# Kernel tuning notes

Hardware: AMD Instinct MI355X
Metric: run time of the kernel (lower is better)

The kernel has to match this reference:

```python
import jax, jax.numpy as jnp
import numpy as np

N = 4_194_304          # number of samples
NUM_TIMES = 2048       # number of distinct (integer) event times


def setup_inputs() -> dict:
    key = jax.random.key(0)
    k1, k2, k3 = jax.random.split(key, 3)
    hazard_ratio = jax.random.normal(k1, (N, 1), dtype=jnp.float32)
    durations = jax.random.randint(k2, (N,), 0, NUM_TIMES, dtype=jnp.int32)
    events = jax.random.randint(k3, (N,), 0, 2, dtype=jnp.int32)
    return {"hazard_ratio": hazard_ratio, "durations": durations, "events": events}


def _cox_efron_loss(hazard_ratio, durations, events):
    """Vectorized Efron-tie Cox PH loss; same math as the nested-loop torch code.

    Original per unique event time t with n tied events:
        loss += sum_k hr_k  -  sum_{k=0}^{n-1} log( sum_{d_i>=t} e^{hr_i} - (k/n) * sum_{tied} e^{hr} )
    which we evaluate per-event-sample using its rank k among ties at its time.
    """
    hr = hazard_ratio.reshape(-1)                       # [N]  (squeeze(-1))
    e = events.astype(hr.dtype)                         # [N] 0/1 floats
    exp_hr = jnp.exp(hr)

    # Per-time aggregates (time ids are 0..NUM_TIMES-1)
    s = jax.ops.segment_sum(exp_hr, durations, num_segments=NUM_TIMES)        # sum e^hr at time d
    R = jnp.cumsum(s[::-1])[::-1]                                             # R[t] = sum_{d>=t} e^hr  (at-risk)
    T = jax.ops.segment_sum(exp_hr * e, durations, num_segments=NUM_TIMES)    # tied-event sum at time t
    n = jax.ops.segment_sum(e, durations, num_segments=NUM_TIMES)             # # tied events at time t

    # Rank of each event sample among the tied events at its time (0-indexed).
    order = jnp.argsort(durations)
    d_s = durations[order]
    e_s = e[order]
    cs = jnp.cumsum(e_s)                                # running event count
    is_start = jnp.concatenate([jnp.array([True]), d_s[1:] != d_s[:-1]])
    # cs - e_s at a segment start equals the event count before the segment;
    # carry it forward with a running max (offsets are nondecreasing, fillers are -1).
    start_val = jnp.where(is_start, cs - e_s, -1.0)
    offset = jax.lax.cummax(start_val)
    rank = cs - offset - 1.0                            # in {0..n-1} for event samples

    n_i = jnp.maximum(n[d_s], 1.0)                      # safe for non-event rows (masked below)
    corr = jnp.log(R[d_s] - (rank / n_i) * T[d_s])      # Efron correction term per event
    corr_sum = jnp.sum(jnp.where(e_s > 0, corr, 0.0))

    loss = jnp.sum(hr * e) - corr_sum
    return -loss / (jnp.sum(e) + 1e-7)


def reference(hazard_ratio, durations, events):
    return _cox_efron_loss(hazard_ratio, durations, events)
```

## Files before the change

kernel.cpp:

```cpp
#include <hip/hip_runtime.h>

#define NT 2048
#define HB 256
#define HT 1024
#define RB 256
#define RT 1024
#define EB 128
#define ET 1024

#define SC      4096.0f
#define INV_SC  (1.0 / 4096.0)
#define TM26    ((1u << 26) - 1)

typedef unsigned long long u64;
typedef unsigned u32;

__device__ __forceinline__ double wave_reduce(double v) {
#pragma unroll
    for (int o = 32; o > 0; o >>= 1) v += __shfl_down(v, o, 64);
    return v;
}

__global__ __launch_bounds__(HT) void k_hist(
    const float* __restrict__ hr, const int* __restrict__ dur,
    const int* __restrict__ ev, int n,
    u32* __restrict__ s0_part, u32* __restrict__ tn_part,
    double* __restrict__ hrE_part, double* __restrict__ eCnt_part,
    unsigned* __restrict__ counter)
{
    __shared__ u32    loc[2][2 * NT];
    __shared__ double redH[HT / 64], redC[HT / 64];

    const int tid = threadIdx.x, bid = blockIdx.x;
    if (bid == 0 && tid == 0) *counter = 0u;

    for (int i = tid; i < 2 * NT; i += HT) { loc[0][i] = 0u; loc[1][i] = 0u; }
    __syncthreads();

    u32* img = loc[(tid >> 6) & 1];

    float hrE = 0.f;
    int   ec  = 0;
    const int stride = HB * HT;
    const int nv = n >> 2;
    const float4* hr4 = (const float4*)hr;
    const int4*   d4p = (const int4*)dur;
    const int4*   e4p = (const int4*)ev;

    auto process = [&](const float4& h, const int4& d, const int4& e) {
        float hh[4] = { h.x, h.y, h.z, h.w };
        int   dd[4] = { d.x, d.y, d.z, d.w };
        int   ee[4] = { e.x, e.y, e.z, e.w };
        u32 val[4]; int idx[4];
#pragma unroll
        for (int u = 0; u < 4; ++u) {
            float eh = __expf(hh[u]);
            val[u] = (u32)(eh * SC + 0.5f) + ((u32)ee[u] << 26);
            idx[u] = dd[u] + (ee[u] << 11);
        }
#pragma unroll
        for (int u = 0; u < 4; ++u)
            atomicAdd(&img[idx[u]], val[u]);
#pragma unroll
        for (int u = 0; u < 4; ++u) {
            hrE += hh[u] * (float)ee[u];
            ec  += ee[u];
        }
    };

    int i = bid * HT + tid;
    if (i < nv) {
        float4 h_c = hr4[i];
        int4   d_c = d4p[i];
        int4   e_c = e4p[i];
        for (i += stride; i < nv; i += stride) {
            float4 h_n = hr4[i];
            int4   d_n = d4p[i];
            int4   e_n = e4p[i];
            process(h_c, d_c, e_c);
            h_c = h_n; d_c = d_n; e_c = e_n;
        }
        process(h_c, d_c, e_c);
    }
    for (int j = (nv << 2) + bid * HT + tid; j < n; j += stride) {
        float h = hr[j]; int d = dur[j]; int e = ev[j];
        float eh = __expf(h);
        atomicAdd(&loc[(tid >> 6) & 1][d + (e << 11)],
                  (u32)(eh * SC + 0.5f) + ((u32)e << 26));
        hrE += h * (float)e;
        ec  += e;
    }
    __syncthreads();

    const size_t base = (size_t)bid * NT;
    for (int k = tid; k < NT; k += HT) {
        s0_part[base + k] = loc[0][k] + loc[1][k];
        u32 a = loc[0][NT + k], b = loc[1][NT + k];
        tn_part[base + k] = (((a >> 26) + (b >> 26)) << 26)
                          + ((a & TM26) + (b & TM26));
    }

    double hrEd = wave_reduce((double)hrE);
    double ecd  = wave_reduce((double)ec);
    if ((tid & 63) == 0) { redH[tid >> 6] = hrEd; redC[tid >> 6] = ecd; }
    __syncthreads();
    if (tid == 0) {
        double hh = 0.0, cc = 0.0;
#pragma unroll
        for (int w = 0; w < HT / 64; ++w) { hh += redH[w]; cc += redC[w]; }
        hrE_part[bid]  = hh;
        eCnt_part[bid] = cc;
    }
}

__global__ __launch_bounds__(RT) void k_reduce(
    const u32* __restrict__ s0_part, const u32* __restrict__ tn_part,
    double* __restrict__ s_fin, double* __restrict__ T_fin,
    unsigned* __restrict__ n_fin)
{
    __shared__ u64      rs[128][8];
    __shared__ u64      rt[128][8];
    __shared__ unsigned rn[128][8];
    __shared__ u64      ps[8][2], pt[8][2];
    __shared__ unsigned pn[8][2];

    const int bi = threadIdx.x & 7;
    const int jg = threadIdx.x >> 3;
    const int t  = blockIdx.x * 8 + bi;

    u64 s = 0ull, T = 0ull;
    unsigned c = 0u;
#pragma unroll
    for (int m = 0; m < HB / 128; ++m) {
        int j = jg + (m << 7);
        size_t idx = (size_t)j * NT + t;
        s += s0_part[idx];
        u32 v = tn_part[idx];
        T += v & TM26;
        c += v >> 26;
    }
    rs[jg][bi] = s; rt[jg][bi] = T; rn[jg][bi] = c;
    __syncthreads();

    const int wv  = threadIdx.x >> 6;
    const int l   = threadIdx.x & 63;
    const int bin = wv >> 1;
    const int hf  = wv & 1;
    u64 S  = rs[hf * 64 + l][bin];
    u64 TT = rt[hf * 64 + l][bin];
    u64 C  = rn[hf * 64 + l][bin];
#pragma unroll
    for (int o = 32; o > 0; o >>= 1) {
        S  += __shfl_down(S,  o, 64);
        TT += __shfl_down(TT, o, 64);
        C  += __shfl_down(C,  o, 64);
    }
    if (l == 0) { ps[bin][hf] = S; pt[bin][hf] = TT; pn[bin][hf] = (unsigned)C; }
    __syncthreads();
    if (threadIdx.x < 8) {
        int b = threadIdx.x;
        u64 S2  = ps[b][0] + ps[b][1];
        u64 TT2 = pt[b][0] + pt[b][1];
        unsigned C2 = pn[b][0] + pn[b][1];
        int tt = blockIdx.x * 8 + b;
        s_fin[tt] = (double)(S2 + TT2) * INV_SC;
        T_fin[tt] = (double)TT2 * INV_SC;
        n_fin[tt] = C2;
    }
}

__global__ __launch_bounds__(ET) void k_scan_efron_final(
    const double* __restrict__ s_fin, const double* __restrict__ T_fin,
    const unsigned* __restrict__ n_fin,
    double* __restrict__ corr_part, const double* __restrict__ hrE_part,
    const double* __restrict__ eCnt_part,
    unsigned* __restrict__ counter, float* __restrict__ out)
{
    __shared__ double sa[NT];
    __shared__ double sb[NT];
    __shared__ double red[16];
    __shared__ unsigned is_last;

    const int tid = threadIdx.x, bid = blockIdx.x;

    for (int i = tid; i < NT; i += ET) sa[i] = s_fin[i];
    __syncthreads();
    double* cur = sa;
    double* nxt = sb;
    for (int off = 1; off < NT; off <<= 1) {
        for (int i = tid; i < NT; i += ET) {
            double v = cur[i];
            if (i + off < NT) v += cur[i + off];
            nxt[i] = v;
        }
        __syncthreads();
        double* tmp = cur; cur = nxt; nxt = tmp;
    }

    const int wv = tid >> 6;
    const int l  = tid & 63;
    const int t  = bid * 16 + wv;
    unsigned nt = n_fin[t];
    double acc = 0.0;
    if (nt > 0) {
        double Rt = cur[t];
        double Tt = T_fin[t];
        double inv = 1.0 / (double)nt;
        for (unsigned k = l; k < nt; k += 64)
            acc += (double)logf((float)(Rt - (double)k * inv * Tt));
    }
    acc = wave_reduce(acc);
    if (l == 0) red[wv] = acc;
    __syncthreads();
    if (tid == 0) {
        double c = 0.0;
#pragma unroll
        for (int m = 0; m < 16; ++m) c += red[m];
        corr_part[bid] = c;
    }
    __syncthreads();

    if (tid == 0) {
        __threadfence();
        unsigned ticket = atomicAdd(counter, 1u);
        is_last = (ticket == EB - 1) ? 1u : 0u;
    }
    __syncthreads();
    if (is_last) {
        __threadfence();
        __shared__ double redA[16], redB[16], redC[16];
        double a = (tid < EB) ? corr_part[tid] : 0.0;
        double h = 0.0, c = 0.0;
        if (tid < HB) { h = hrE_part[tid]; c = eCnt_part[tid]; }
        a = wave_reduce(a); h = wave_reduce(h); c = wave_reduce(c);
        if ((tid & 63) == 0) { redA[tid >> 6] = a; redB[tid >> 6] = h; redC[tid >> 6] = c; }
        __syncthreads();
        if (tid == 0) {
            double A = 0.0, H = 0.0, C = 0.0;
#pragma unroll
            for (int w = 0; w < 16; ++w) { A += redA[w]; H += redB[w]; C += redC[w]; }
            out[0] = (float)(-(H - A) / (C + 1e-7));
        }
    }
}

extern "C" void kernel_launch(void* const* d_in, const int* in_sizes, int n_in,
                              void* d_out, int out_size, void* d_ws, size_t ws_size,
                              hipStream_t stream)
{
    const float* hr  = (const float*)d_in[0];
    const int*   dur = (const int*)d_in[1];
    const int*   ev  = (const int*)d_in[2];
    int n = in_sizes[1];

    char* ws = (char*)d_ws;
    u32*      s0_part   = (u32*)ws;
    u32*      tn_part   = (u32*)(ws + (size_t)2 * 1024 * 1024);
    char*     p         = ws + (size_t)4 * 1024 * 1024;
    double*   s_fin     = (double*)p;          p += NT * 8;
    double*   T_fin     = (double*)p;          p += NT * 8;
    unsigned* n_fin     = (unsigned*)p;        p += NT * 4;
    double*   corr_part = (double*)p;          p += EB * 8;
    double*   hrE_part  = (double*)p;          p += HB * 8;
    double*   eCnt_part = (double*)p;          p += HB * 8;
    unsigned* counter   = (unsigned*)p;

    hipLaunchKernelGGL(k_hist, dim3(HB), dim3(HT), 0, stream,
                       hr, dur, ev, n, s0_part, tn_part, hrE_part, eCnt_part, counter);
    hipLaunchKernelGGL(k_reduce, dim3(RB), dim3(RT), 0, stream,
                       s0_part, tn_part, s_fin, T_fin, n_fin);
    hipLaunchKernelGGL(k_scan_efron_final, dim3(EB), dim3(ET), 0, stream,
                       s_fin, T_fin, n_fin, corr_part, hrE_part, eCnt_part,
                       counter, (float*)d_out);
}
```

Before: 35.71 us.

## Fuse reduce and scan kernels using per-block chunk sums for suffix offsets

The histogram kernel now also writes per-block sums over 128 chunks of 16 time bins. The separate reduce and scan+Efron kernels are merged into one finish kernel. Each of its 128 blocks reduces its own 16 bins across all partial histograms, builds a 128-entry suffix scan of chunk totals, and adds a local suffix within its chunk to get the at-risk sums. This removes one kernel launch, the intermediate global arrays, and the 2048-wide scan repeated in every block. The cost is an extra chunk reduction in the histogram kernel and a reduction over all chunk partials in every finish block.

After: 39.60 us. 1.11x slower.

```diff
diff --git a/kernel.cpp b/kernel.cpp
--- a/kernel.cpp
+++ b/kernel.cpp
@@ -3,10 +3,9 @@
 #define NT 2048
 #define HB 256
 #define HT 1024
-#define RB 256
-#define RT 1024
-#define EB 128
-#define ET 1024
+#define NC 128
+#define FB 128
+#define FT 1024
 
 #define SC      4096.0f
 #define INV_SC  (1.0 / 4096.0)
@@ -25,6 +24,7 @@
     const float* __restrict__ hr, const int* __restrict__ dur,
     const int* __restrict__ ev, int n,
     u32* __restrict__ s0_part, u32* __restrict__ tn_part,
+    u64* __restrict__ chunk_part,
     double* __restrict__ hrE_part, double* __restrict__ eCnt_part,
     unsigned* __restrict__ counter)
 {
@@ -100,6 +100,18 @@
                           + ((a & TM26) + (b & TM26));
     }
 
+    if (tid < NC) {
+        const int t0 = tid * (NT / NC);
+        u64 s = 0ull;
+#pragma unroll
+        for (int j = 0; j < NT / NC; ++j) {
+            int t = t0 + j;
+            s += (u64)loc[0][t] + (u64)loc[1][t]
+               + (u64)(loc[0][NT + t] & TM26) + (u64)(loc[1][NT + t] & TM26);
+        }
+        chunk_part[(size_t)bid * NC + tid] = s;
+    }
+
     double hrEd = wave_reduce((double)hrE);
     double ecd  = wave_reduce((double)ec);
     if ((tid & 63) == 0) { redH[tid >> 6] = hrEd; redC[tid >> 6] = ecd; }
@@ -113,104 +125,109 @@
     }
 }
 
-__global__ __launch_bounds__(RT) void k_reduce(
+__global__ __launch_bounds__(FT) void k_finish(
     const u32* __restrict__ s0_part, const u32* __restrict__ tn_part,
-    double* __restrict__ s_fin, double* __restrict__ T_fin,
-    unsigned* __restrict__ n_fin)
-{
-    __shared__ u64      rs[128][8];
-    __shared__ u64      rt[128][8];
-    __shared__ unsigned rn[128][8];
-    __shared__ u64      ps[8][2], pt[8][2];
-    __shared__ unsigned pn[8][2];
-
-    const int bi = threadIdx.x & 7;
-    const int jg = threadIdx.x >> 3;
-    const int t  = blockIdx.x * 8 + bi;
-
-    u64 s = 0ull, T = 0ull;
-    unsigned c = 0u;
-#pragma unroll
-    for (int m = 0; m < HB / 128; ++m) {
-        int j = jg + (m << 7);
-        size_t idx = (size_t)j * NT + t;
-        s += s0_part[idx];
-        u32 v = tn_part[idx];
-        T += v & TM26;
-        c += v >> 26;
-    }
-    rs[jg][bi] = s; rt[jg][bi] = T; rn[jg][bi] = c;
-    __syncthreads();
-
-    const int wv  = threadIdx.x >> 6;
-    const int l   = threadIdx.x & 63;
-    const int bin = wv >> 1;
-    const int hf  = wv & 1;
-    u64 S  = rs[hf * 64 + l][bin];
-    u64 TT = rt[hf * 64 + l][bin];
-    u64 C  = rn[hf * 64 + l][bin];
-#pragma unroll
-    for (int o = 32; o > 0; o >>= 1) {
-        S  += __shfl_down(S,  o, 64);
-        TT += __shfl_down(TT, o, 64);
-        C  += __shfl_down(C,  o, 64);
-    }
-    if (l == 0) { ps[bin][hf] = S; pt[bin][hf] = TT; pn[bin][hf] = (unsigned)C; }
-    __syncthreads();
-    if (threadIdx.x < 8) {
-        int b = threadIdx.x;
-        u64 S2  = ps[b][0] + ps[b][1];
-        u64 TT2 = pt[b][0] + pt[b][1];
-        unsigned C2 = pn[b][0] + pn[b][1];
-        int tt = blockIdx.x * 8 + b;
-        s_fin[tt] = (double)(S2 + TT2) * INV_SC;
-        T_fin[tt] = (double)TT2 * INV_SC;
-        n_fin[tt] = C2;
-    }
-}
-
-__global__ __launch_bounds__(ET) void k_scan_efron_final(
-    const double* __restrict__ s_fin, const double* __restrict__ T_fin,
-    const unsigned* __restrict__ n_fin,
-    double* __restrict__ corr_part, const double* __restrict__ hrE_part,
-    const double* __restrict__ eCnt_part,
+    const u64* __restrict__ chunk_part,
+    const double* __restrict__ hrE_part, const double* __restrict__ eCnt_part,
+    double* __restrict__ corr_part,
     unsigned* __restrict__ counter, float* __restrict__ out)
 {
-    __shared__ double sa[NT];
-    __shared__ double sb[NT];
+    __shared__ u64 rs[64][16];
+    __shared__ u64 rt[64][16];
+    __shared__ u32 rn[64][16];
+    __shared__ u64 sbin[16];
+    __shared__ u64 tbin[16];
+    __shared__ u32 nbin[16];
+    __shared__ u64 cstage[8][NC];
+    __shared__ u64 ctA[NC], ctB[NC];
+    __shared__ u64 Rfx[16];
     __shared__ double red[16];
     __shared__ unsigned is_last;
 
     const int tid = threadIdx.x, bid = blockIdx.x;
 
-    for (int i = tid; i < NT; i += ET) sa[i] = s_fin[i];
-    __syncthreads();
-    double* cur = sa;
-    double* nxt = sb;
-    for (int off = 1; off < NT; off <<= 1) {
-        for (int i = tid; i < NT; i += ET) {
-            double v = cur[i];
-            if (i + off < NT) v += cur[i + off];
-            nxt[i] = v;
-        }
-        __syncthreads();
-        double* tmp = cur; cur = nxt; nxt = tmp;
-    }
-
-    const int wv = tid >> 6;
-    const int l  = tid & 63;
-    const int t  = bid * 16 + wv;
-    unsigned nt = n_fin[t];
-    double acc = 0.0;
-    if (nt > 0) {
-        double Rt = cur[t];
-        double Tt = T_fin[t];
-        double inv = 1.0 / (double)nt;
-        for (unsigned k = l; k < nt; k += 64)
-            acc += (double)logf((float)(Rt - (double)k * inv * Tt));
-    }
-    acc = wave_reduce(acc);
-    if (l == 0) red[wv] = acc;
+    {
+        const int bi = tid & 15;
+        const int jg = tid >> 4;
+        const int t  = bid * 16 + bi;
+        u64 s = 0ull, T = 0ull; u32 c = 0u;
+#pragma unroll
+        for (int r = 0; r < 4; ++r) {
+            int row = jg * 4 + r;
+            size_t idx = (size_t)row * NT + t;
+            s += s0_part[idx];
+            u32 v = tn_part[idx];
+            T += v & TM26;
+            c += v >> 26;
+        }
+        rs[jg][bi] = s; rt[jg][bi] = T; rn[jg][bi] = c;
+    }
+    __syncthreads();
+    {
+        const int wv = tid >> 6;
+        const int l  = tid & 63;
+        u64 S = rs[l][wv], TT = rt[l][wv], C = rn[l][wv];
+#pragma unroll
+        for (int o = 32; o > 0; o >>= 1) {
+            S  += __shfl_down(S,  o, 64);
+            TT += __shfl_down(TT, o, 64);
+            C  += __shfl_down(C,  o, 64);
+        }
+        if (l == 0) { sbin[wv] = S + TT; tbin[wv] = TT; nbin[wv] = (u32)C; }
+    }
+
+    {
+        const int c = tid & (NC - 1);
+        const int g = tid >> 7;
+        u64 acc = 0ull;
+        for (int r = g; r < HB; r += 8)
+            acc += chunk_part[(size_t)r * NC + c];
+        cstage[g][c] = acc;
+    }
+    __syncthreads();
+    if (tid < NC) {
+        u64 tot = 0ull;
+#pragma unroll
+        for (int g = 0; g < 8; ++g) tot += cstage[g][tid];
+        ctA[tid] = tot;
+    }
+    __syncthreads();
+
+    {
+        u64* cur = ctA;
+        u64* nxt = ctB;
+        for (int off = 1; off < NC; off <<= 1) {
+            if (tid < NC) {
+                u64 v = cur[tid];
+                if (tid + off < NC) v += cur[tid + off];
+                nxt[tid] = v;
+            }
+            __syncthreads();
+            u64* tmp = cur; cur = nxt; nxt = tmp;
+        }
+        if (tid < 16) {
+            u64 r = (bid + 1 < NC) ? cur[bid + 1] : 0ull;
+            for (int j = 15; j >= (int)tid; --j) r += sbin[j];
+            Rfx[tid] = r;
+        }
+    }
+    __syncthreads();
+
+    {
+        const int wv = tid >> 6;
+        const int l  = tid & 63;
+        u32 nt = nbin[wv];
+        double acc = 0.0;
+        if (nt > 0) {
+            double Rt = (double)Rfx[wv] * INV_SC;
+            double Tt = (double)tbin[wv] * INV_SC;
+            double inv = 1.0 / (double)nt;
+            for (u32 k = l; k < nt; k += 64)
+                acc += (double)logf((float)(Rt - (double)k * inv * Tt));
+        }
+        acc = wave_reduce(acc);
+        if (l == 0) red[wv] = acc;
+    }
     __syncthreads();
     if (tid == 0) {
         double c = 0.0;
@@ -223,13 +240,13 @@
     if (tid == 0) {
         __threadfence();
         unsigned ticket = atomicAdd(counter, 1u);
-        is_last = (ticket == EB - 1) ? 1u : 0u;
+        is_last = (ticket == FB - 1) ? 1u : 0u;
     }
     __syncthreads();
     if (is_last) {
         __threadfence();
         __shared__ double redA[16], redB[16], redC[16];
-        double a = (tid < EB) ? corr_part[tid] : 0.0;
+        double a = (tid < FB) ? corr_part[tid] : 0.0;
         double h = 0.0, c = 0.0;
         if (tid < HB) { h = hrE_part[tid]; c = eCnt_part[tid]; }
         a = wave_reduce(a); h = wave_reduce(h); c = wave_reduce(c);
@@ -254,22 +271,19 @@
     int n = in_sizes[1];
 
     char* ws = (char*)d_ws;
-    u32*      s0_part   = (u32*)ws;
-    u32*      tn_part   = (u32*)(ws + (size_t)2 * 1024 * 1024);
-    char*     p         = ws + (size_t)4 * 1024 * 1024;
-    double*   s_fin     = (double*)p;          p += NT * 8;
-    double*   T_fin     = (double*)p;          p += NT * 8;
-    unsigned* n_fin     = (unsigned*)p;        p += NT * 4;
-    double*   corr_part = (double*)p;          p += EB * 8;
-    double*   hrE_part  = (double*)p;          p += HB * 8;
-    double*   eCnt_part = (double*)p;          p += HB * 8;
-    unsigned* counter   = (unsigned*)p;
+    u32*      s0_part    = (u32*)ws;
+    u32*      tn_part    = (u32*)(ws + (size_t)2 * 1024 * 1024);
+    char*     p          = ws + (size_t)4 * 1024 * 1024;
+    u64*      chunk_part = (u64*)p;            p += (size_t)HB * NC * 8;
+    double*   corr_part  = (double*)p;         p += FB * 8;
+    double*   hrE_part   = (double*)p;         p += HB * 8;
+    double*   eCnt_part  = (double*)p;         p += HB * 8;
+    unsigned* counter    = (unsigned*)p;
 
     hipLaunchKernelGGL(k_hist, dim3(HB), dim3(HT), 0, stream,
-                       hr, dur, ev, n, s0_part, tn_part, hrE_part, eCnt_part, counter);
-    hipLaunchKernelGGL(k_reduce, dim3(RB), dim3(RT), 0, stream,
-                       s0_part, tn_part, s_fin, T_fin, n_fin);
-    hipLaunchKernelGGL(k_scan_efron_final, dim3(EB), dim3(ET), 0, stream,
-                       s_fin, T_fin, n_fin, corr_part, hrE_part, eCnt_part,
-                       counter, (float*)d_out);
-}
+                       hr, dur, ev, n, s0_part, tn_part, chunk_part,
+                       hrE_part, eCnt_part, counter);
+    hipLaunchKernelGGL(k_finish, dim3(FB), dim3(FT), 0, stream,
+                       s0_part, tn_part, chunk_part, hrE_part, eCnt_part,
+                       corr_part, counter, (float*)d_out);
+}
```

## Stream histogram inputs into LDS via async global_load_lds double buffering

Applied to the files above, without the earlier changes.

The histogram kernel now gives each block a contiguous slab of 16K elements and streams it into LDS in four 4K chunks with global_load_lds DMA. The loads are double-buffered and ordered with explicit vmcnt waits, so the next chunk is in flight while the current one is binned. This replaces the grid-strided float4 register prefetch and is meant to hide memory latency and use larger contiguous reads. It adds LDS pressure (about 80KB per block) and relies on hand-placed waitcnt values, and any tail beyond HB*PERBLK is handled by a scalar loop.

Result: slower. 36.90 us (+3.3%).

```diff
diff --git a/kernel.cpp b/kernel.cpp
--- a/kernel.cpp
+++ b/kernel.cpp
@@ -3,6 +3,9 @@
 #define NT 2048
 #define HB 256
 #define HT 1024
+#define CH 4096
+#define NCH 4
+#define PERBLK (CH * NCH)
 #define RB 256
 #define RT 1024
 #define EB 128
@@ -14,6 +17,13 @@
 
 typedef unsigned long long u64;
 typedef unsigned u32;
+
+typedef const __attribute__((address_space(1))) void gvoid;
+typedef __attribute__((address_space(3))) void svoid;
+
+__device__ __forceinline__ void dma16(const void* g, void* l) {
+    __builtin_amdgcn_global_load_lds((gvoid*)g, (svoid*)l, 16, 0, 0);
+}
 
 __device__ __forceinline__ double wave_reduce(double v) {
 #pragma unroll
@@ -28,26 +38,28 @@
     double* __restrict__ hrE_part, double* __restrict__ eCnt_part,
     unsigned* __restrict__ counter)
 {
-    __shared__ u32    loc[2][2 * NT];
+    __shared__ u32    img[2][2 * NT];
+    __shared__ float  hrb[2][CH];
+    __shared__ int    dub[2][CH];
+    __shared__ int    evb[2][CH];
     __shared__ double redH[HT / 64], redC[HT / 64];
 
-    const int tid = threadIdx.x, bid = blockIdx.x;
+    const int tid  = threadIdx.x, bid = blockIdx.x;
+    const int w    = tid >> 6;
+    const int lane = tid & 63;
     if (bid == 0 && tid == 0) *counter = 0u;
 
-    for (int i = tid; i < 2 * NT; i += HT) { loc[0][i] = 0u; loc[1][i] = 0u; }
-    __syncthreads();
-
-    u32* img = loc[(tid >> 6) & 1];
-
+    for (int i = tid; i < 2 * NT; i += HT) { img[0][i] = 0u; img[1][i] = 0u; }
+    __syncthreads();
+
+    u32* myimg = img[w & 1];
     float hrE = 0.f;
     int   ec  = 0;
-    const int stride = HB * HT;
-    const int nv = n >> 2;
-    const float4* hr4 = (const float4*)hr;
-    const int4*   d4p = (const int4*)dur;
-    const int4*   e4p = (const int4*)ev;
-
-    auto process = [&](const float4& h, const int4& d, const int4& e) {
+
+    const size_t base = (size_t)bid * PERBLK;
+    const int    seg  = w * (CH / 16);
+
+    auto process4 = [&](float4 h, int4 d, int4 e) {
         float hh[4] = { h.x, h.y, h.z, h.w };
         int   dd[4] = { d.x, d.y, d.z, d.w };
         int   ee[4] = { e.x, e.y, e.z, e.w };
@@ -60,7 +72,7 @@
         }
 #pragma unroll
         for (int u = 0; u < 4; ++u)
-            atomicAdd(&img[idx[u]], val[u]);
+            atomicAdd(&myimg[idx[u]], val[u]);
 #pragma unroll
         for (int u = 0; u < 4; ++u) {
             hrE += hh[u] * (float)ee[u];
@@ -68,36 +80,56 @@
         }
     };
 
-    int i = bid * HT + tid;
-    if (i < nv) {
-        float4 h_c = hr4[i];
-        int4   d_c = d4p[i];
-        int4   e_c = e4p[i];
-        for (i += stride; i < nv; i += stride) {
-            float4 h_n = hr4[i];
-            int4   d_n = d4p[i];
-            int4   e_n = e4p[i];
-            process(h_c, d_c, e_c);
-            h_c = h_n; d_c = d_n; e_c = e_n;
-        }
-        process(h_c, d_c, e_c);
-    }
-    for (int j = (nv << 2) + bid * HT + tid; j < n; j += stride) {
+    if (base + PERBLK <= (size_t)n) {
+        auto ISSUE = [&](int c) {
+            const int b = c & 1;
+            const size_t off = base + (size_t)c * CH + seg + (size_t)lane * 4;
+            dma16(hr  + off, &hrb[b][seg]);
+            dma16(dur + off, &dub[b][seg]);
+            dma16(ev  + off, &evb[b][seg]);
+        };
+        ISSUE(0);
+#pragma unroll
+        for (int c = 0; c < NCH; ++c) {
+            if (c + 1 < NCH) {
+                ISSUE(c + 1);
+                asm volatile("s_waitcnt vmcnt(3)" ::: "memory");
+            } else {
+                asm volatile("s_waitcnt vmcnt(0)" ::: "memory");
+            }
+            __builtin_amdgcn_sched_barrier(0);
+            const int b = c & 1;
+            const int t4 = seg + lane * 4;
+            float4 h = *(const float4*)&hrb[b][t4];
+            int4   d = *(const int4*)&dub[b][t4];
+            int4   e = *(const int4*)&evb[b][t4];
+            process4(h, d, e);
+        }
+    } else {
+        for (size_t j = base + tid; j < (size_t)n && j < base + PERBLK; j += HT) {
+            float h = hr[j]; int d = dur[j]; int e = ev[j];
+            float eh = __expf(h);
+            atomicAdd(&myimg[d + (e << 11)], (u32)(eh * SC + 0.5f) + ((u32)e << 26));
+            hrE += h * (float)e;
+            ec  += e;
+        }
+    }
+    for (size_t j = (size_t)HB * PERBLK + (size_t)bid * HT + tid; j < (size_t)n;
+         j += (size_t)HB * HT) {
         float h = hr[j]; int d = dur[j]; int e = ev[j];
         float eh = __expf(h);
-        atomicAdd(&loc[(tid >> 6) & 1][d + (e << 11)],
-                  (u32)(eh * SC + 0.5f) + ((u32)e << 26));
+        atomicAdd(&myimg[d + (e << 11)], (u32)(eh * SC + 0.5f) + ((u32)e << 26));
         hrE += h * (float)e;
         ec  += e;
     }
     __syncthreads();
 
-    const size_t base = (size_t)bid * NT;
+    const size_t prow = (size_t)bid * NT;
     for (int k = tid; k < NT; k += HT) {
-        s0_part[base + k] = loc[0][k] + loc[1][k];
-        u32 a = loc[0][NT + k], b = loc[1][NT + k];
-        tn_part[base + k] = (((a >> 26) + (b >> 26)) << 26)
-                          + ((a & TM26) + (b & TM26));
+        s0_part[prow + k] = img[0][k] + img[1][k];
+        u32 a = img[0][NT + k], b2 = img[1][NT + k];
+        tn_part[prow + k] = (((a >> 26) + (b2 >> 26)) << 26)
+                          + ((a & TM26) + (b2 & TM26));
     }
 
     double hrEd = wave_reduce((double)hrE);
@@ -107,7 +139,7 @@
     if (tid == 0) {
         double hh = 0.0, cc = 0.0;
 #pragma unroll
-        for (int w = 0; w < HT / 64; ++w) { hh += redH[w]; cc += redC[w]; }
+        for (int m = 0; m < HT / 64; ++m) { hh += redH[m]; cc += redC[m]; }
         hrE_part[bid]  = hh;
         eCnt_part[bid] = cc;
     }
@@ -238,7 +270,7 @@
         if (tid == 0) {
             double A = 0.0, H = 0.0, C = 0.0;
 #pragma unroll
-            for (int w = 0; w < 16; ++w) { A += redA[w]; H += redB[w]; C += redC[w]; }
+            for (int m = 0; m < 16; ++m) { A += redA[m]; H += redB[m]; C += redC[m]; }
             out[0] = (float)(-(H - A) / (C + 1e-7));
         }
     }
```

## Split histogram into pack pass producing 32-bit packed samples, then atomic histogram

Applied to the files above, without the earlier changes.

Adds a separate high-occupancy kernel that reads hazard, duration and event arrays, computes exp and packs a 20-bit fixed-point value, an 11-bit time and an event bit into one word. It also computes the per-block hrE and event-count partials. The histogram kernel then reads only the packed array and does shared-memory atomics, so its loop carries less load and no exp work. The aim is to spread the streaming and exp work over more blocks while keeping the atomic phase lean. In exchange it writes and re-reads a 16 MB intermediate, adds a launch, and coarsens the fixed-point scale with clamping, which reduces precision and could saturate large exp values.

After: 43.90 us. +22.9%, slower.

```diff
diff --git a/kernel.cpp b/kernel.cpp
--- a/kernel.cpp
+++ b/kernel.cpp
@@ -1,6 +1,8 @@
 #include <hip/hip_runtime.h>
 
 #define NT 2048
+#define WB 2048
+#define WT 256
 #define HB 256
 #define HT 1024
 #define RB 256
@@ -8,8 +10,9 @@
 #define EB 128
 #define ET 1024
 
-#define SC      4096.0f
-#define INV_SC  (1.0 / 4096.0)
+#define SC      2048.0f
+#define INV_SC  (1.0 / 2048.0)
+#define FXMAX   0xFFFFFu
 #define TM26    ((1u << 26) - 1)
 
 typedef unsigned long long u64;
@@ -21,74 +24,111 @@
     return v;
 }
 
-__global__ __launch_bounds__(HT) void k_hist(
+__device__ __forceinline__ u32 pack1(float h, int d, int e) {
+    u32 fx = (u32)(__expf(h) * SC + 0.5f);
+    fx = fx > FXMAX ? FXMAX : fx;
+    return fx | ((u32)d << 20) | ((u32)e << 31);
+}
+
+__global__ __launch_bounds__(WT) void k_pack(
     const float* __restrict__ hr, const int* __restrict__ dur,
     const int* __restrict__ ev, int n,
-    u32* __restrict__ s0_part, u32* __restrict__ tn_part,
+    u32* __restrict__ packed,
     double* __restrict__ hrE_part, double* __restrict__ eCnt_part,
     unsigned* __restrict__ counter)
 {
-    __shared__ u32    loc[2][2 * NT];
-    __shared__ double redH[HT / 64], redC[HT / 64];
-
+    __shared__ double redH[WT / 64], redC[WT / 64];
     const int tid = threadIdx.x, bid = blockIdx.x;
     if (bid == 0 && tid == 0) *counter = 0u;
 
-    for (int i = tid; i < 2 * NT; i += HT) { loc[0][i] = 0u; loc[1][i] = 0u; }
-    __syncthreads();
-
-    u32* img = loc[(tid >> 6) & 1];
-
-    float hrE = 0.f;
-    int   ec  = 0;
-    const int stride = HB * HT;
-    const int nv = n >> 2;
     const float4* hr4 = (const float4*)hr;
     const int4*   d4p = (const int4*)dur;
     const int4*   e4p = (const int4*)ev;
-
-    auto process = [&](const float4& h, const int4& d, const int4& e) {
-        float hh[4] = { h.x, h.y, h.z, h.w };
-        int   dd[4] = { d.x, d.y, d.z, d.w };
-        int   ee[4] = { e.x, e.y, e.z, e.w };
+    uint4*        pk4 = (uint4*)packed;
+    const int nv = n >> 2;
+    const int stride = WB * WT;
+
+    float hrE = 0.f;
+    int   ec  = 0;
+    for (int i = bid * WT + tid; i < nv; i += stride) {
+        float4 h = hr4[i];
+        int4   d = d4p[i];
+        int4   e = e4p[i];
+        uint4 o;
+        o.x = pack1(h.x, d.x, e.x);
+        o.y = pack1(h.y, d.y, e.y);
+        o.z = pack1(h.z, d.z, e.z);
+        o.w = pack1(h.w, d.w, e.w);
+        pk4[i] = o;
+        hrE += h.x * (float)e.x + h.y * (float)e.y
+             + h.z * (float)e.z + h.w * (float)e.w;
+        ec  += e.x + e.y + e.z + e.w;
+    }
+    for (int j = (nv << 2) + bid * WT + tid; j < n; j += stride) {
+        float h = hr[j]; int d = dur[j]; int e = ev[j];
+        packed[j] = pack1(h, d, e);
+        hrE += h * (float)e;
+        ec  += e;
+    }
+
+    double hrEd = wave_reduce((double)hrE);
+    double ecd  = wave_reduce((double)ec);
+    if ((tid & 63) == 0) { redH[tid >> 6] = hrEd; redC[tid >> 6] = ecd; }
+    __syncthreads();
+    if (tid == 0) {
+        double hh = 0.0, cc = 0.0;
+#pragma unroll
+        for (int w = 0; w < WT / 64; ++w) { hh += redH[w]; cc += redC[w]; }
+        hrE_part[bid]  = hh;
+        eCnt_part[bid] = cc;
+    }
+}
+
+__global__ __launch_bounds__(HT) void k_hist(
+    const u32* __restrict__ packed, int n,
+    u32* __restrict__ s0_part, u32* __restrict__ tn_part)
+{
+    __shared__ u32 loc[2][2 * NT];
+
+    const int tid = threadIdx.x, bid = blockIdx.x;
+    for (int i = tid; i < 2 * NT; i += HT) { loc[0][i] = 0u; loc[1][i] = 0u; }
+    __syncthreads();
+
+    u32* img = loc[(tid >> 6) & 1];
+    const uint4* pk4 = (const uint4*)packed;
+    const int nv = n >> 2;
+    const int stride = HB * HT;
+
+    auto process = [&](uint4 v) {
+        u32 vv[4] = { v.x, v.y, v.z, v.w };
         u32 val[4]; int idx[4];
 #pragma unroll
         for (int u = 0; u < 4; ++u) {
-            float eh = __expf(hh[u]);
-            val[u] = (u32)(eh * SC + 0.5f) + ((u32)ee[u] << 26);
-            idx[u] = dd[u] + (ee[u] << 11);
+            u32 fx = vv[u] & FXMAX;
+            u32 d  = (vv[u] >> 20) & 0x7FFu;
+            u32 e  = vv[u] >> 31;
+            val[u] = fx + (e << 26);
+            idx[u] = (int)(d + (e << 11));
         }
 #pragma unroll
         for (int u = 0; u < 4; ++u)
             atomicAdd(&img[idx[u]], val[u]);
-#pragma unroll
-        for (int u = 0; u < 4; ++u) {
-            hrE += hh[u] * (float)ee[u];
-            ec  += ee[u];
-        }
     };
 
     int i = bid * HT + tid;
     if (i < nv) {
-        float4 h_c = hr4[i];
-        int4   d_c = d4p[i];
-        int4   e_c = e4p[i];
+        uint4 c = pk4[i];
         for (i += stride; i < nv; i += stride) {
-            float4 h_n = hr4[i];
-            int4   d_n = d4p[i];
-            int4   e_n = e4p[i];
-            process(h_c, d_c, e_c);
-            h_c = h_n; d_c = d_n; e_c = e_n;
+            uint4 nx = pk4[i];
+            process(c);
+            c = nx;
         }
-        process(h_c, d_c, e_c);
+        process(c);
     }
     for (int j = (nv << 2) + bid * HT + tid; j < n; j += stride) {
-        float h = hr[j]; int d = dur[j]; int e = ev[j];
-        float eh = __expf(h);
-        atomicAdd(&loc[(tid >> 6) & 1][d + (e << 11)],
-                  (u32)(eh * SC + 0.5f) + ((u32)e << 26));
-        hrE += h * (float)e;
-        ec  += e;
+        u32 v = packed[j];
+        u32 fx = v & FXMAX, d = (v >> 20) & 0x7FFu, e = v >> 31;
+        atomicAdd(&loc[(tid >> 6) & 1][d + (e << 11)], fx + (e << 26));
     }
     __syncthreads();
 
@@ -98,18 +138,6 @@
         u32 a = loc[0][NT + k], b = loc[1][NT + k];
         tn_part[base + k] = (((a >> 26) + (b >> 26)) << 26)
                           + ((a & TM26) + (b & TM26));
-    }
-
-    double hrEd = wave_reduce((double)hrE);
-    double ecd  = wave_reduce((double)ec);
-    if ((tid & 63) == 0) { redH[tid >> 6] = hrEd; redC[tid >> 6] = ecd; }
-    __syncthreads();
-    if (tid == 0) {
-        double hh = 0.0, cc = 0.0;
-#pragma unroll
-        for (int w = 0; w < HT / 64; ++w) { hh += redH[w]; cc += redC[w]; }
-        hrE_part[bid]  = hh;
-        eCnt_part[bid] = cc;
     }
 }
 
@@ -231,7 +259,7 @@
         __shared__ double redA[16], redB[16], redC[16];
         double a = (tid < EB) ? corr_part[tid] : 0.0;
         double h = 0.0, c = 0.0;
-        if (tid < HB) { h = hrE_part[tid]; c = eCnt_part[tid]; }
+        for (int m = tid; m < WB; m += ET) { h += hrE_part[m]; c += eCnt_part[m]; }
         a = wave_reduce(a); h = wave_reduce(h); c = wave_reduce(c);
         if ((tid & 63) == 0) { redA[tid >> 6] = a; redB[tid >> 6] = h; redC[tid >> 6] = c; }
         __syncthreads();
@@ -256,17 +284,20 @@
     char* ws = (char*)d_ws;
     u32*      s0_part   = (u32*)ws;
     u32*      tn_part   = (u32*)(ws + (size_t)2 * 1024 * 1024);
-    char*     p         = ws + (size_t)4 * 1024 * 1024;
+    u32*      packed    = (u32*)(ws + (size_t)4 * 1024 * 1024);
+    char*     p         = ws + (size_t)24 * 1024 * 1024;
     double*   s_fin     = (double*)p;          p += NT * 8;
     double*   T_fin     = (double*)p;          p += NT * 8;
     unsigned* n_fin     = (unsigned*)p;        p += NT * 4;
     double*   corr_part = (double*)p;          p += EB * 8;
-    double*   hrE_part  = (double*)p;          p += HB * 8;
-    double*   eCnt_part = (double*)p;          p += HB * 8;
+    double*   hrE_part  = (double*)p;          p += WB * 8;
+    double*   eCnt_part = (double*)p;          p += WB * 8;
     unsigned* counter   = (unsigned*)p;
 
+    hipLaunchKernelGGL(k_pack, dim3(WB), dim3(WT), 0, stream,
+                       hr, dur, ev, n, packed, hrE_part, eCnt_part, counter);
     hipLaunchKernelGGL(k_hist, dim3(HB), dim3(HT), 0, stream,
-                       hr, dur, ev, n, s0_part, tn_part, hrE_part, eCnt_part, counter);
+                       packed, n, s0_part, tn_part);
     hipLaunchKernelGGL(k_reduce, dim3(RB), dim3(RT), 0, stream,
                        s0_part, tn_part, s_fin, T_fin, n_fin);
     hipLaunchKernelGGL(k_scan_efron_final, dim3(EB), dim3(ET), 0, stream,
```
